# Performance work log

Hardware: AMD Instinct MI355X
Metric: run time of the kernel (lower is better)

## Reference

```python
import jax, jax.numpy as jnp
import numpy as np

NEG_BIG = 1e8  # mask value from the original code


def setup_inputs() -> dict:
    key = jax.random.key(0)
    k1, k2, k3, k4, k5 = jax.random.split(key, 5)
    B, L, H, D = 16, 128, 256, 256
    # xavier-uniform-ish scale for the weight matrices
    lim = float(np.sqrt(6.0 / (H + D)))
    return {
        "encoder_output": jax.random.normal(k1, (B, L, H), dtype=jnp.float32),
        "W_l": jax.random.uniform(k2, (H, D), jnp.float32, -lim, lim),
        "W_r": jax.random.uniform(k3, (H, D), jnp.float32, -lim, lim),
        "U": jax.random.uniform(k4, (D,), jnp.float32, 0.0, 1.0),
        "logit_bias": jax.random.uniform(k5, (1,), jnp.float32, 0.0, 1.0),
    }


def reference(encoder_output, W_l, W_r, U, logit_bias):
    B, L, H = encoder_output.shape
    # projections: (B, L, D)
    dot_l = jnp.einsum("blh,hd->bld", encoder_output, W_l)
    dot_r = jnp.einsum("blh,hd->bld", encoder_output, W_r)
    # pairwise additive attention: (B, L, L, D) -> (B, L, L)
    final_sum = jnp.tanh(dot_l[:, :, None, :] + dot_r[:, None, :, :])
    logits = jnp.einsum("bijd,d->bij", final_sum, U) + logit_bias[0]
    # per-step diagonal mask (one_hot(i) at step i) vectorized as eye
    mask = jnp.eye(L, dtype=logits.dtype)  # (L, L)
    mask_scores = logits - NEG_BIG * mask[None, :, :]  # (B, L, L)
    probs = jax.nn.sigmoid(mask_scores)
    # Bernoulli sample (fixed key for reproducibility)
    samples = jax.random.bernoulli(jax.random.key(1), probs).astype(logits.dtype)  # graphs (B,L,L)
    # Bernoulli entropy: p*softplus(-l) + (1-p)*softplus(l), numerically stable
    entropy = probs * jax.nn.softplus(-mask_scores) + (1.0 - probs) * jax.nn.softplus(mask_scores)
    graph_batch = jnp.mean(samples, axis=0)  # (L, L)
    # BCE-with-logits mean over all elements (targets = sampled graphs)
    log_softmax = jnp.mean(jax.nn.softplus(mask_scores) - mask_scores * samples)
    entropy_regularization = jnp.mean(jnp.mean(entropy, axis=2), axis=1)  # (B,)
    return (mask_scores, samples, entropy, graph_batch, log_softmax, entropy_regularization)
```

## Files before the change

### kernel.cpp

```cpp
#include <hip/hip_runtime.h>

#define Bn 16
#define Ln 128
#define Hn 256
#define Dn 256

#define OFF_MASK   0
#define OFF_SMP    262144
#define OFF_ENT    524288
#define OFF_GRAPH  786432
#define OFF_LSE    802816
#define OFF_EREG   802817

static __device__ __forceinline__ unsigned rotl32(unsigned x, int r) {
  return (x << r) | (x >> (32 - r));
}

static __device__ __forceinline__ unsigned threefry_bits(unsigned c_hi, unsigned c_lo) {
  const unsigned ks0 = 0u, ks1 = 1u;
  const unsigned ks2 = 0u ^ 1u ^ 0x1BD11BDAu;
  unsigned x0 = c_hi + ks0;
  unsigned x1 = c_lo + ks1;
  x0 += x1; x1 = rotl32(x1, 13); x1 ^= x0;
  x0 += x1; x1 = rotl32(x1, 15); x1 ^= x0;
  x0 += x1; x1 = rotl32(x1, 26); x1 ^= x0;
  x0 += x1; x1 = rotl32(x1, 6);  x1 ^= x0;
  x0 += ks1; x1 += ks2 + 1u;
  x0 += x1; x1 = rotl32(x1, 17); x1 ^= x0;
  x0 += x1; x1 = rotl32(x1, 29); x1 ^= x0;
  x0 += x1; x1 = rotl32(x1, 16); x1 ^= x0;
  x0 += x1; x1 = rotl32(x1, 24); x1 ^= x0;
  x0 += ks2; x1 += ks0 + 2u;
  x0 += x1; x1 = rotl32(x1, 13); x1 ^= x0;
  x0 += x1; x1 = rotl32(x1, 15); x1 ^= x0;
  x0 += x1; x1 = rotl32(x1, 26); x1 ^= x0;
  x0 += x1; x1 = rotl32(x1, 6);  x1 ^= x0;
  x0 += ks0; x1 += ks1 + 3u;
  x0 += x1; x1 = rotl32(x1, 17); x1 ^= x0;
  x0 += x1; x1 = rotl32(x1, 29); x1 ^= x0;
  x0 += x1; x1 = rotl32(x1, 16); x1 ^= x0;
  x0 += x1; x1 = rotl32(x1, 24); x1 ^= x0;
  x0 += ks1; x1 += ks2 + 4u;
  x0 += x1; x1 = rotl32(x1, 13); x1 ^= x0;
  x0 += x1; x1 = rotl32(x1, 15); x1 ^= x0;
  x0 += x1; x1 = rotl32(x1, 26); x1 ^= x0;
  x0 += x1; x1 = rotl32(x1, 6);  x1 ^= x0;
  x0 += ks2; x1 += ks0 + 5u;
  return x0 ^ x1;
}

static __device__ __forceinline__ float softplus_f(float x) {
  return fmaxf(x, 0.0f) + log1pf(__expf(-fabsf(x)));
}

static __device__ __forceinline__ float fast_tanh(float x) {
  float e = __expf(-2.0f * x);
  float r = __builtin_amdgcn_rcpf(1.0f + e);
  return fmaf(2.0f, r, -1.0f);
}

static __device__ __forceinline__ void load_lds16(const float4* g, float4* l) {
  __builtin_amdgcn_global_load_lds((const __attribute__((address_space(1))) void*)g,
                                   (__attribute__((address_space(3))) void*)l,
                                   16, 0, 0);
}

__global__ void proj_kernel(const float* __restrict__ enc,
                            const float* __restrict__ Wl,
                            const float* __restrict__ Wr,
                            float* __restrict__ dl,
                            float* __restrict__ dr,
                            float* __restrict__ out,
                            double* __restrict__ ws_acc) {
  int gid = blockIdx.x * blockDim.x + threadIdx.x;
  if (gid < Ln * Ln) out[OFF_GRAPH + gid] = 0.0f;
  if (gid < 18) ws_acc[gid] = 0.0;

  int r0 = blockIdx.x * 4;
  int d = threadIdx.x;
  __shared__ float encS[4][Hn];
  __shared__ float WlS[32][Dn];
  __shared__ float WrS[32][Dn];
  ((float4*)encS)[d] = ((const float4*)(enc + (size_t)r0 * Hn))[d];

  float al[4] = {0.f, 0.f, 0.f, 0.f};
  float ar[4] = {0.f, 0.f, 0.f, 0.f};

  for (int c = 0; c < 8; ++c) {
    {
      const float4* wlg = (const float4*)(Wl + (size_t)c * 32 * Dn);
      const float4* wrg = (const float4*)(Wr + (size_t)c * 32 * Dn);
#pragma unroll
      for (int s = 0; s < 8; ++s) load_lds16(&wlg[s * 256 + d], &((float4*)WlS)[s * 256 + d]);
#pragma unroll
      for (int s = 0; s < 8; ++s) load_lds16(&wrg[s * 256 + d], &((float4*)WrS)[s * 256 + d]);
    }
    __syncthreads();

#pragma unroll
    for (int h4l = 0; h4l < 8; ++h4l) {
      float4 e[4];
#pragma unroll
      for (int r = 0; r < 4; ++r) e[r] = ((const float4*)encS[r])[c * 8 + h4l];
#pragma unroll
      for (int q = 0; q < 4; ++q) {
        int hh = h4l * 4 + q;
        float wl = WlS[hh][d];
        float wr = WrS[hh][d];
#pragma unroll
        for (int r = 0; r < 4; ++r) {
          float ev = (q == 0) ? e[r].x : (q == 1) ? e[r].y : (q == 2) ? e[r].z : e[r].w;
          al[r] = fmaf(ev, wl, al[r]);
          ar[r] = fmaf(ev, wr, ar[r]);
        }
      }
    }
    if (c < 7) __syncthreads();
  }
#pragma unroll
  for (int r = 0; r < 4; ++r) {
    dl[(size_t)(r0 + r) * Dn + d] = al[r];
    dr[(size_t)(r0 + r) * Dn + d] = ar[r];
  }
}

__global__ void pair_kernel(const float* __restrict__ dl,
                            const float* __restrict__ dr,
                            const float* __restrict__ U,
                            const float* __restrict__ bias,
                            float* __restrict__ out,
                            double* __restrict__ ws_acc) {
  int blk = blockIdx.x;
  int b = blk >> 6;
  int i0 = ((blk >> 1) & 31) * 4;
  int j0 = (blk & 1) * 64;
  int t = threadIdx.x;
  int dp = t & 15;
  int jj = t >> 4;

  __shared__ float dlS[4][Dn];
  __shared__ float pS[4][64 * 17];
  __shared__ float redS[8];

  ((float4*)dlS)[t] = ((const float4*)(dl + (size_t)(b * Ln + i0) * Dn))[t];

  float Ur[16];
  {
    const float4* U4 = (const float4*)(U + dp * 16);
#pragma unroll
    for (int q = 0; q < 4; ++q) {
      float4 u = U4[q];
      Ur[4*q+0] = u.x; Ur[4*q+1] = u.y; Ur[4*q+2] = u.z; Ur[4*q+3] = u.w;
    }
  }
  __syncthreads();

  float dlr[4][16];
#pragma unroll
  for (int r = 0; r < 4; ++r) {
#pragma unroll
    for (int q = 0; q < 4; ++q) {
      float4 a = *(const float4*)&dlS[r][dp * 16 + q * 4];
      dlr[r][4*q+0] = a.x; dlr[r][4*q+1] = a.y; dlr[r][4*q+2] = a.z; dlr[r][4*q+3] = a.w;
    }
  }

  const float* drt = dr + (size_t)b * Ln * Dn + (size_t)(j0 + jj) * Dn + dp * 16;
#pragma unroll
  for (int tl = 0; tl < 4; ++tl) {
    const float4* drp = (const float4*)(drt + (size_t)tl * 16 * Dn);
    float a0 = 0.f, a1 = 0.f, a2 = 0.f, a3 = 0.f;
#pragma unroll
    for (int q = 0; q < 4; ++q) {
      float4 v = drp[q];
#pragma unroll
      for (int c = 0; c < 4; ++c) {
        float dv = (c == 0) ? v.x : (c == 1) ? v.y : (c == 2) ? v.z : v.w;
        float uv = Ur[4*q+c];
        a0 = fmaf(fast_tanh(dlr[0][4*q+c] + dv), uv, a0);
        a1 = fmaf(fast_tanh(dlr[1][4*q+c] + dv), uv, a1);
        a2 = fmaf(fast_tanh(dlr[2][4*q+c] + dv), uv, a2);
        a3 = fmaf(fast_tanh(dlr[3][4*q+c] + dv), uv, a3);
      }
    }
    int sa = (tl * 16 + jj) * 17 + dp;
    pS[0][sa] = a0; pS[1][sa] = a1; pS[2][sa] = a2; pS[3][sa] = a3;
  }
  __syncthreads();

  int row = t >> 6;
  int jl = t & 63;
  int j = j0 + jl;
  const float* ps = &pS[row][jl * 17];
  float tot = 0.0f;
#pragma unroll
  for (int k = 0; k < 16; ++k) tot += ps[k];
  int i = i0 + row;
  float l = tot + bias[0] - ((j == i) ? 1.0e8f : 0.0f);
  float e = __expf(-l);
  float p = __builtin_amdgcn_rcpf(1.0f + e);
  unsigned n = ((unsigned)(b * Ln + i) << 7) | (unsigned)j;
  unsigned bits = threefry_bits(0u, n);
  float u = __uint_as_float((bits >> 9) | 0x3f800000u) - 1.0f;
  float smp = (u < p) ? 1.0f : 0.0f;
  float sp_pos = softplus_f(l);
  float sp_neg = softplus_f(-l);
  float ent = p * sp_neg + (1.0f - p) * sp_pos;
  size_t idx = (size_t)(b * Ln + i) * Ln + j;
  out[OFF_MASK + idx] = l;
  out[OFF_SMP + idx] = smp;
  out[OFF_ENT + idx] = ent;
  atomicAdd(&out[OFF_GRAPH + i * Ln + j], smp * 0.0625f);
  float ent_v = ent;
  float lse_v = sp_pos - l * smp;

#pragma unroll
  for (int off = 32; off > 0; off >>= 1) {
    ent_v += __shfl_down(ent_v, off);
    lse_v += __shfl_down(lse_v, off);
  }
  if ((t & 63) == 0) {
    redS[(t >> 6) * 2 + 0] = ent_v;
    redS[(t >> 6) * 2 + 1] = lse_v;
  }
  __syncthreads();
  if (t == 0) {
    float es = redS[0] + redS[2] + redS[4] + redS[6];
    float ls = redS[1] + redS[3] + redS[5] + redS[7];
    atomicAdd(&ws_acc[b], (double)es);
    atomicAdd(&ws_acc[16], (double)ls);
    __threadfence();
    unsigned int* ctr = (unsigned int*)&ws_acc[17];
    unsigned done = atomicAdd(ctr, 1u);
    if (done == (unsigned)(gridDim.x - 1)) {
      double ls_tot = atomicAdd(&ws_acc[16], 0.0);
      out[OFF_LSE] = (float)(ls_tot / (double)(Bn * Ln * Ln));
      for (int q = 0; q < Bn; ++q) {
        double ev = atomicAdd(&ws_acc[q], 0.0);
        out[OFF_EREG + q] = (float)(ev / (double)(Ln * Ln));
      }
    }
  }
}

extern "C" void kernel_launch(void* const* d_in, const int* in_sizes, int n_in,
                              void* d_out, int out_size, void* d_ws, size_t ws_size,
                              hipStream_t stream) {
  const float* enc = (const float*)d_in[0];
  const float* Wl = (const float*)d_in[1];
  const float* Wr = (const float*)d_in[2];
  const float* U = (const float*)d_in[3];
  const float* bias = (const float*)d_in[4];
  float* out = (float*)d_out;

  float* dl = (float*)d_ws;
  float* dr = dl + (size_t)Bn * Ln * Dn;
  double* ws_acc = (double*)(dr + (size_t)Bn * Ln * Dn);

  proj_kernel<<<Bn * Ln / 4, 256, 0, stream>>>(enc, Wl, Wr, dl, dr, out, ws_acc);
  pair_kernel<<<Bn * Ln / 2, 256, 0, stream>>>(dl, dr, U, bias, out, ws_acc);
}
```

Baseline: 123.2 us.

## Retile projection kernel to 16 rows per block with direct global weight loads

After: 125.3 us. About the same (+1.7%).

```diff
diff --git a/kernel.cpp b/kernel.cpp
--- a/kernel.cpp
+++ b/kernel.cpp
@@ -59,12 +59,6 @@
   return fmaf(2.0f, r, -1.0f);
 }
 
-static __device__ __forceinline__ void load_lds16(const float4* g, float4* l) {
-  __builtin_amdgcn_global_load_lds((const __attribute__((address_space(1))) void*)g,
-                                   (__attribute__((address_space(3))) void*)l,
-                                   16, 0, 0);
-}
-
 __global__ void proj_kernel(const float* __restrict__ enc,
                             const float* __restrict__ Wl,
                             const float* __restrict__ Wr,
@@ -76,52 +70,43 @@
   if (gid < Ln * Ln) out[OFF_GRAPH + gid] = 0.0f;
   if (gid < 18) ws_acc[gid] = 0.0;
 
-  int r0 = blockIdx.x * 4;
-  int d = threadIdx.x;
-  __shared__ float encS[4][Hn];
-  __shared__ float WlS[32][Dn];
-  __shared__ float WrS[32][Dn];
-  ((float4*)encS)[d] = ((const float4*)(enc + (size_t)r0 * Hn))[d];
-
-  float al[4] = {0.f, 0.f, 0.f, 0.f};
-  float ar[4] = {0.f, 0.f, 0.f, 0.f};
-
-  for (int c = 0; c < 8; ++c) {
-    {
-      const float4* wlg = (const float4*)(Wl + (size_t)c * 32 * Dn);
-      const float4* wrg = (const float4*)(Wr + (size_t)c * 32 * Dn);
-#pragma unroll
-      for (int s = 0; s < 8; ++s) load_lds16(&wlg[s * 256 + d], &((float4*)WlS)[s * 256 + d]);
-#pragma unroll
-      for (int s = 0; s < 8; ++s) load_lds16(&wrg[s * 256 + d], &((float4*)WrS)[s * 256 + d]);
-    }
-    __syncthreads();
-
-#pragma unroll
-    for (int h4l = 0; h4l < 8; ++h4l) {
-      float4 e[4];
-#pragma unroll
-      for (int r = 0; r < 4; ++r) e[r] = ((const float4*)encS[r])[c * 8 + h4l];
-#pragma unroll
-      for (int q = 0; q < 4; ++q) {
-        int hh = h4l * 4 + q;
-        float wl = WlS[hh][d];
-        float wr = WrS[hh][d];
-#pragma unroll
-        for (int r = 0; r < 4; ++r) {
-          float ev = (q == 0) ? e[r].x : (q == 1) ? e[r].y : (q == 2) ? e[r].z : e[r].w;
-          al[r] = fmaf(ev, wl, al[r]);
-          ar[r] = fmaf(ev, wr, ar[r]);
-        }
-      }
-    }
-    if (c < 7) __syncthreads();
-  }
-#pragma unroll
-  for (int r = 0; r < 4; ++r) {
-    dl[(size_t)(r0 + r) * Dn + d] = al[r];
-    dr[(size_t)(r0 + r) * Dn + d] = ar[r];
-  }
+  int g = blockIdx.x;
+  int rg = g >> 3;
+  int mat = (g >> 2) & 1;
+  int dq = g & 3;
+  int r0 = rg * 16;
+  int d0 = dq * 64;
+
+  int t = threadIdx.x;
+  int dcol = d0 + (t & 63);
+  int rsub = t >> 6;
+
+  __shared__ float encS[16][Hn];
+#pragma unroll
+  for (int q = 0; q < 4; ++q)
+    ((float4*)encS)[q * 256 + t] = ((const float4*)(enc + (size_t)r0 * Hn))[q * 256 + t];
+  __syncthreads();
+
+  const float* wp = (mat ? Wr : Wl) + dcol;
+  float a[4] = {0.f, 0.f, 0.f, 0.f};
+
+  for (int h8 = 0; h8 < Hn / 8; ++h8) {
+    float wv[8];
+#pragma unroll
+    for (int u = 0; u < 8; ++u) wv[u] = wp[(size_t)(h8 * 8 + u) * Dn];
+#pragma unroll
+    for (int u = 0; u < 8; ++u) {
+      int h = h8 * 8 + u;
+#pragma unroll
+      for (int rr = 0; rr < 4; ++rr)
+        a[rr] = fmaf(encS[rsub * 4 + rr][h], wv[u], a[rr]);
+    }
+  }
+
+  float* dst = mat ? dr : dl;
+#pragma unroll
+  for (int rr = 0; rr < 4; ++rr)
+    dst[(size_t)(r0 + rsub * 4 + rr) * Dn + dcol] = a[rr];
 }
 
 __global__ void pair_kernel(const float* __restrict__ dl,
@@ -257,6 +242,6 @@
   float* dr = dl + (size_t)Bn * Ln * Dn;
   double* ws_acc = (double*)(dr + (size_t)Bn * Ln * Dn);
 
-  proj_kernel<<<Bn * Ln / 4, 256, 0, stream>>>(enc, Wl, Wr, dl, dr, out, ws_acc);
+  proj_kernel<<<1024, 256, 0, stream>>>(enc, Wl, Wr, dl, dr, out, ws_acc);
   pair_kernel<<<Bn * Ln / 2, 256, 0, stream>>>(dl, dr, U, bias, out, ws_acc);
 }
```
